# Kernel tuning notes

Hardware: AMD Instinct MI355X
Metric: run time of the kernel (lower is better)

The kernel has to match this reference:

```python
import jax, jax.numpy as jnp
import numpy as np

NUM_EMBEDDINGS = 1024
EMBEDDING_DIM = 256


def setup_inputs() -> dict:
    key = jax.random.key(0)
    kx, kw = jax.random.split(key)
    x = jax.random.normal(kx, (64, 32, 32, EMBEDDING_DIM), dtype=jnp.float32)
    # nn.Embedding default init: N(0, 1)
    embedding_weight = jax.random.normal(kw, (NUM_EMBEDDINGS, EMBEDDING_DIM), dtype=jnp.float32)
    return {"x": x, "embedding_weight": embedding_weight}


def reference(x, embedding_weight):
    D = embedding_weight.shape[1]
    x_flat = x.reshape(-1, D)  # [N, D]
    distances = (
        jnp.sum(x_flat * x_flat, axis=1, keepdims=True)
        + jnp.sum(embedding_weight * embedding_weight, axis=1)
        - 2.0 * jnp.matmul(x_flat, embedding_weight.T)
    )
    indices = jnp.argmin(distances, axis=1)  # [N]
    quantized = embedding_weight[indices].reshape(x.shape)
    return quantized, indices
```

## Files before the change

### kernel.cpp

```cpp
#include <hip/hip_runtime.h>


#define K_EMB  1024
#define D_DIM  256
#define N_ROWS 65536

typedef unsigned int u32;
typedef unsigned long long u64;
typedef __attribute__((ext_vector_type(8)))  _Float16 f16x8;
typedef __attribute__((ext_vector_type(4)))  _Float16 f16x4;
typedef __attribute__((ext_vector_type(16))) float    f32x16;

__device__ __forceinline__ u32 f32_sortable(float f) {
    u32 u = __float_as_uint(f);
    return u ^ ((u32)((int)u >> 31) | 0x80000000u);
}
__device__ __forceinline__ float f32_unsort(u32 u) {
    u32 v = (u & 0x80000000u) ? (u ^ 0x80000000u) : ~u;
    return __uint_as_float(v);
}

#define GLDS(gp, lp) __builtin_amdgcn_global_load_lds( \
    (const __attribute__((address_space(1))) void*)(gp), \
    (__attribute__((address_space(3))) void*)(lp), 16, 0, 0)

__global__ void vq_prep(const float* __restrict__ emb,
                        _Float16* __restrict__ ehi,
                        u32* __restrict__ cn2c,
                        float* __restrict__ cnormf) {
    int gid = blockIdx.x * 256 + threadIdx.x;
    int code = gid >> 6, lane = gid & 63;
    float4 v = ((const float4*)(emb + (size_t)code * D_DIM))[lane];
    f16x4 hv = {(_Float16)v.x, (_Float16)v.y, (_Float16)v.z, (_Float16)v.w};
    ((f16x4*)(ehi + (size_t)code * D_DIM))[lane] = hv;
    float s = v.x * v.x + v.y * v.y + v.z * v.z + v.w * v.w;
    #pragma unroll
    for (int off = 32; off > 0; off >>= 1) s += __shfl_down(s, off, 64);
    if (lane == 0) {
        float cn = 0.5f * s;
        cnormf[code] = cn;
        _Float16 ch = (_Float16)cn;
        _Float16 cl = (_Float16)(cn - (float)ch);
        union { _Float16 hh[2]; u32 uu; } pk;
        pk.hh[0] = (_Float16)(-(float)ch);
        pk.hh[1] = (_Float16)(-(float)cl);
        cn2c[code] = pk.uu;
    }
}

__global__ __launch_bounds__(512, 4) void vq_main(
    const float* __restrict__ x, const float* __restrict__ emb,
    const _Float16* __restrict__ eh, const u32* __restrict__ cn2c,
    const float* __restrict__ cnormf,
    float* __restrict__ outq, float* __restrict__ outi)
{
    __shared__ _Float16 T[2][2][8192];
    __shared__ u32 CNs[1024];
    __shared__ u32 xchg[2][128][3];
    __shared__ int winners[128];

    const int t = threadIdx.x, w = t >> 6, lane = t & 63;
    const int m = lane & 31, kh = lane >> 5;
    const int p = w >> 1;
    const int h = w & 1;
    const int blkrow = blockIdx.x * 128;
    const int kh4 = kh * 4;

    auto stage = [&](int c) {
        _Float16* dstb = &T[c & 1][h][0];
        const _Float16* srcb = eh + (size_t)(h * 512 + c * 32 + m) * D_DIM + kh * 8;
        #pragma unroll
        for (int i = 0; i < 4; i++) {
            int r = p * 4 + i;
            GLDS(srcb + r * 16, dstb + r * 512);
        }
    };

    stage(0);

    CNs[t] = cn2c[t];
    CNs[t + 512] = cn2c[t + 512];

    f16x8 bh[16];
    {
        char* xb = (char*)&T[1][0][0];
        #pragma unroll
        for (int k = 0; k < 2; k++) {
            #pragma unroll
            for (int i = 0; i < 8; i++) {
                int row = i * 8 + w;
                float4 v = *(const float4*)(
                    x + (size_t)(blkrow + k * 64 + row) * D_DIM + lane * 4);
                f16x4 hv = {(_Float16)v.x, (_Float16)v.y,
                            (_Float16)v.z, (_Float16)v.w};
                u32 byte = (u32)(row * 512 + lane * 8) ^ ((u32)(row & 7) << 4);
                *(f16x4*)(xb + byte) = hv;
            }
            __syncthreads();
            if ((p >> 1) == k) {
                int lr = (p & 1) * 32 + m;
                #pragma unroll
                for (int s = 0; s < 16; s++) {
                    u32 byte = (u32)(lr * 512 + s * 32 + kh * 16)
                             ^ ((u32)(lr & 7) << 4);
                    bh[s] = *(const f16x8*)(xb + byte);
                }
            }
            __syncthreads();
        }
    }
    f16x8 xe = {};
    if (kh == 0) { xe[0] = (_Float16)1.0f; xe[1] = (_Float16)1.0f; }

    u32 A1 = 0, A2 = 0, A3 = 0;

    auto t3 = [](u32& c1, u32& c2, u32& c3, u32 pv) {
        u32 u2 = c1 < pv ? c1 : pv;
        u32 u3 = c2 < pv ? c2 : pv;
        c1 = c1 > pv ? c1 : pv;
        c2 = u2 > c2 ? u2 : c2;
        c3 = u3 > c3 ? u3 : c3;
    };

    for (int c = 0; c < 16; ++c) {
        __builtin_amdgcn_sched_barrier(0);
        __builtin_amdgcn_s_barrier();
        if (c < 15) {
            stage(c + 1);
            asm volatile("s_waitcnt vmcnt(4)" ::: "memory");
        } else {
            asm volatile("s_waitcnt vmcnt(0)" ::: "memory");
        }
        __builtin_amdgcn_sched_barrier(0);
        __builtin_amdgcn_s_barrier();

        const f16x8* Af = (const f16x8*)&T[c & 1][h][0];
        union { u32 uu; _Float16 hh[2]; } uv;
        uv.uu = CNs[h * 512 + c * 32 + m];
        f16x8 e = {};
        e[0] = uv.hh[0]; e[1] = uv.hh[1];
        f32x16 a = {};
        __builtin_amdgcn_s_setprio(1);
        #pragma unroll
        for (int s = 0; s < 16; s++) {
            f16x8 fa = Af[(2 * s + kh) * 32 + m];
            a = __builtin_amdgcn_mfma_f32_32x32x16_f16(fa, bh[s], a, 0, 0, 0);
        }
        a = __builtin_amdgcn_mfma_f32_32x32x16_f16(e, xe, a, 0, 0, 0);
        __builtin_amdgcn_s_setprio(0);

        const u32 sbase = (u32)(h * 512 + c * 32) + kh4;
        #pragma unroll
        for (int r = 0; r < 16; r++) {
            u32 code = sbase + (r & 3) + 8 * (r >> 2);
            u32 pk = (f32_sortable(a[r]) & 0xFFFFFC00u) | code;
            t3(A1, A2, A3, pk);
        }
    }

    {
        u32 q1 = (u32)__shfl_xor((int)A1, 32, 64);
        u32 q2 = (u32)__shfl_xor((int)A2, 32, 64);
        u32 q3 = (u32)__shfl_xor((int)A3, 32, 64);
        t3(A1, A2, A3, q1); t3(A1, A2, A3, q2); t3(A1, A2, A3, q3);
    }

    if (kh == 0) {
        int ra = p * 32 + m;
        xchg[h][ra][0] = A1; xchg[h][ra][1] = A2; xchg[h][ra][2] = A3;
    }
    __syncthreads();

    const int lr = w * 16 + (lane & 15);
    u32 c1 = 0, c2 = 0, c3 = 0;
    #pragma unroll
    for (int hh = 0; hh < 2; hh++) {
        t3(c1, c2, c3, xchg[hh][lr][0]);
        t3(c1, c2, c3, xchg[hh][lr][1]);
        t3(c1, c2, c3, xchg[hh][lr][2]);
    }

    float s1f = f32_unsort(c1), s2f = f32_unsort(c2), s3f = f32_unsort(c3);
    u32 i1 = c1 & 1023u, i2 = c2 & 1023u, i3 = c3 & 1023u;
    const bool act = lane < 16;
    bool need = (s1f - s2f) <= 0.25f;
    if (act && !need) winners[lr] = (int)i1;
    u64 mask = __ballot(act && need);
    while (mask) {
        int r = __ffsll((unsigned long long)mask) - 1;
        mask &= mask - 1;
        int row = blkrow + w * 16 + r;
        u32 d1 = (u32)__shfl((int)i1, r, 64);
        u32 d2 = (u32)__shfl((int)i2, r, 64);
        u32 d3 = (u32)__shfl((int)i3, r, 64);
        float g3 = __shfl(s1f - s3f, r, 64);
        int ncand = (g3 <= 0.25f) ? 3 : 2;
        float4 xv = ((const float4*)(x + (size_t)row * D_DIM))[lane];
        float bs = -3.0e38f; int bi = 0x7fffffff;
        u32 cand[3] = {d1, d2, d3};
        for (int q = 0; q < ncand; q++) {
            int ccd = (int)cand[q];
            float4 ev = ((const float4*)(emb + (size_t)ccd * D_DIM))[lane];
            float d = xv.x * ev.x + xv.y * ev.y + xv.z * ev.z + xv.w * ev.w;
            #pragma unroll
            for (int dd = 1; dd < 64; dd <<= 1) d += __shfl_xor(d, dd, 64);
            float sc = d - cnormf[ccd];
            if (sc > bs || (sc == bs && ccd < bi)) { bs = sc; bi = ccd; }
        }
        if (lane == 0) winners[w * 16 + r] = bi;
    }

    if (act) outi[blkrow + lr] = (float)winners[lr];
    #pragma unroll 8
    for (int r = 0; r < 16; r++) {
        int idx = winners[w * 16 + r];
        int row = blkrow + w * 16 + r;
        float4 qv = ((const float4*)(emb + (size_t)idx * D_DIM))[lane];
        ((float4*)(outq + (size_t)row * D_DIM))[lane] = qv;
    }
}

extern "C" void kernel_launch(void* const* d_in, const int* in_sizes, int n_in,
                              void* d_out, int out_size, void* d_ws, size_t ws_size,
                              hipStream_t stream) {
    const float* x   = (const float*)d_in[0];
    const float* emb = (const float*)d_in[1];
    float* outq = (float*)d_out;
    float* outi = outq + (size_t)N_ROWS * D_DIM;

    _Float16* ehi = (_Float16*)d_ws;
    u32* cn2c = (u32*)(ehi + (size_t)K_EMB * D_DIM);
    float* cnormf = (float*)(cn2c + K_EMB);

    vq_prep<<<K_EMB / 4, 256, 0, stream>>>(emb, ehi, cn2c, cnormf);
    vq_main<<<N_ROWS / 128, 512, 0, stream>>>(x, emb, ehi, cn2c, cnormf,
                                              outq, outi);
}
```

Baseline: 155.1 us.

## Software-pipeline MFMA with top-3 selection and use float med3 top-3

Unrolls the codebook chunk loop by two with two accumulators, so the top-3 scan of the previous chunk runs while the MFMAs of the current chunk are issued. The unsigned sortable-key top-3 is replaced by a float top-3 built from fmed3/fmax on the raw float bits with the code index packed into the low mantissa bits, which removes the per-element sortable conversion. The cost is a second 16-float accumulator, which raises register pressure at 4 waves per SIMD, and the float comparison of index-packed values depends on those values not being negative or NaN.

```diff
diff --git a/kernel.cpp b/kernel.cpp
--- a/kernel.cpp
+++ b/kernel.cpp
@@ -10,15 +10,6 @@
 typedef __attribute__((ext_vector_type(8)))  _Float16 f16x8;
 typedef __attribute__((ext_vector_type(4)))  _Float16 f16x4;
 typedef __attribute__((ext_vector_type(16))) float    f32x16;
-
-__device__ __forceinline__ u32 f32_sortable(float f) {
-    u32 u = __float_as_uint(f);
-    return u ^ ((u32)((int)u >> 31) | 0x80000000u);
-}
-__device__ __forceinline__ float f32_unsort(u32 u) {
-    u32 v = (u & 0x80000000u) ? (u ^ 0x80000000u) : ~u;
-    return __uint_as_float(v);
-}
 
 #define GLDS(gp, lp) __builtin_amdgcn_global_load_lds( \
     (const __attribute__((address_space(1))) void*)(gp), \
@@ -65,6 +56,7 @@
     const int h = w & 1;
     const int blkrow = blockIdx.x * 128;
     const int kh4 = kh * 4;
+    const float NEGINF = __uint_as_float(0xFF800000u);
 
     auto stage = [&](int c) {
         _Float16* dstb = &T[c & 1][h][0];
@@ -112,34 +104,22 @@
     f16x8 xe = {};
     if (kh == 0) { xe[0] = (_Float16)1.0f; xe[1] = (_Float16)1.0f; }
 
-    u32 A1 = 0, A2 = 0, A3 = 0;
-
-    auto t3 = [](u32& c1, u32& c2, u32& c3, u32 pv) {
-        u32 u2 = c1 < pv ? c1 : pv;
-        u32 u3 = c2 < pv ? c2 : pv;
-        c1 = c1 > pv ? c1 : pv;
-        c2 = u2 > c2 ? u2 : c2;
-        c3 = u3 > c3 ? u3 : c3;
-    };
-
-    for (int c = 0; c < 16; ++c) {
-        __builtin_amdgcn_sched_barrier(0);
-        __builtin_amdgcn_s_barrier();
-        if (c < 15) {
-            stage(c + 1);
-            asm volatile("s_waitcnt vmcnt(4)" ::: "memory");
-        } else {
-            asm volatile("s_waitcnt vmcnt(0)" ::: "memory");
-        }
-        __builtin_amdgcn_sched_barrier(0);
-        __builtin_amdgcn_s_barrier();
-
-        const f16x8* Af = (const f16x8*)&T[c & 1][h][0];
+    float B1 = NEGINF, B2 = NEGINF, B3 = NEGINF;
+
+    auto t3f = [](float& c1, float& c2, float& c3, float pv) {
+        float n3 = __builtin_amdgcn_fmed3f(c2, pv, c3);
+        float n2 = __builtin_amdgcn_fmed3f(c1, pv, c2);
+        c1 = fmaxf(c1, pv);
+        c2 = n2; c3 = n3;
+    };
+
+    auto computeMF = [&](int buf, f32x16& a, int c) {
+        const f16x8* Af = (const f16x8*)&T[buf][h][0];
         union { u32 uu; _Float16 hh[2]; } uv;
         uv.uu = CNs[h * 512 + c * 32 + m];
         f16x8 e = {};
         e[0] = uv.hh[0]; e[1] = uv.hh[1];
-        f32x16 a = {};
+        a = (f32x16){};
         __builtin_amdgcn_s_setprio(1);
         #pragma unroll
         for (int s = 0; s < 16; s++) {
@@ -148,42 +128,73 @@
         }
         a = __builtin_amdgcn_mfma_f32_32x32x16_f16(e, xe, a, 0, 0, 0);
         __builtin_amdgcn_s_setprio(0);
-
+    };
+
+    auto top3p = [&](const f32x16& a, int c) {
         const u32 sbase = (u32)(h * 512 + c * 32) + kh4;
         #pragma unroll
         for (int r = 0; r < 16; r++) {
             u32 code = sbase + (r & 3) + 8 * (r >> 2);
-            u32 pk = (f32_sortable(a[r]) & 0xFFFFFC00u) | code;
-            t3(A1, A2, A3, pk);
-        }
-    }
+            u32 bits = (__float_as_uint(a[r]) & 0xFFFFFC00u) | code;
+            t3f(B1, B2, B3, __uint_as_float(bits));
+        }
+    };
+
+    f32x16 accA, accB;
+    for (int cc = 0; cc < 16; cc += 2) {
+        __builtin_amdgcn_sched_barrier(0);
+        __builtin_amdgcn_s_barrier();
+        stage(cc + 1);
+        asm volatile("s_waitcnt vmcnt(4)" ::: "memory");
+        __builtin_amdgcn_sched_barrier(0);
+        __builtin_amdgcn_s_barrier();
+        computeMF(0, accA, cc);
+        if (cc) top3p(accB, cc - 1);
+
+        __builtin_amdgcn_sched_barrier(0);
+        __builtin_amdgcn_s_barrier();
+        if (cc + 2 < 16) {
+            stage(cc + 2);
+            asm volatile("s_waitcnt vmcnt(4)" ::: "memory");
+        } else {
+            asm volatile("s_waitcnt vmcnt(0)" ::: "memory");
+        }
+        __builtin_amdgcn_sched_barrier(0);
+        __builtin_amdgcn_s_barrier();
+        computeMF(1, accB, cc + 1);
+        top3p(accA, cc);
+    }
+    top3p(accB, 15);
 
     {
-        u32 q1 = (u32)__shfl_xor((int)A1, 32, 64);
-        u32 q2 = (u32)__shfl_xor((int)A2, 32, 64);
-        u32 q3 = (u32)__shfl_xor((int)A3, 32, 64);
-        t3(A1, A2, A3, q1); t3(A1, A2, A3, q2); t3(A1, A2, A3, q3);
+        float q1 = __shfl_xor(B1, 32, 64);
+        float q2 = __shfl_xor(B2, 32, 64);
+        float q3 = __shfl_xor(B3, 32, 64);
+        t3f(B1, B2, B3, q1); t3f(B1, B2, B3, q2); t3f(B1, B2, B3, q3);
     }
 
     if (kh == 0) {
         int ra = p * 32 + m;
-        xchg[h][ra][0] = A1; xchg[h][ra][1] = A2; xchg[h][ra][2] = A3;
+        xchg[h][ra][0] = __float_as_uint(B1);
+        xchg[h][ra][1] = __float_as_uint(B2);
+        xchg[h][ra][2] = __float_as_uint(B3);
     }
     __syncthreads();
 
     const int lr = w * 16 + (lane & 15);
-    u32 c1 = 0, c2 = 0, c3 = 0;
+    float c1 = NEGINF, c2 = NEGINF, c3 = NEGINF;
     #pragma unroll
     for (int hh = 0; hh < 2; hh++) {
-        t3(c1, c2, c3, xchg[hh][lr][0]);
-        t3(c1, c2, c3, xchg[hh][lr][1]);
-        t3(c1, c2, c3, xchg[hh][lr][2]);
-    }
-
-    float s1f = f32_unsort(c1), s2f = f32_unsort(c2), s3f = f32_unsort(c3);
-    u32 i1 = c1 & 1023u, i2 = c2 & 1023u, i3 = c3 & 1023u;
+        t3f(c1, c2, c3, __uint_as_float(xchg[hh][lr][0]));
+        t3f(c1, c2, c3, __uint_as_float(xchg[hh][lr][1]));
+        t3f(c1, c2, c3, __uint_as_float(xchg[hh][lr][2]));
+    }
+
+    u32 i1 = __float_as_uint(c1) & 1023u;
+    u32 i2 = __float_as_uint(c2) & 1023u;
+    u32 i3 = __float_as_uint(c3) & 1023u;
     const bool act = lane < 16;
-    bool need = (s1f - s2f) <= 0.25f;
+    bool need = (c1 - c2) <= 0.25f;
     if (act && !need) winners[lr] = (int)i1;
     u64 mask = __ballot(act && need);
     while (mask) {
@@ -193,7 +204,7 @@
         u32 d1 = (u32)__shfl((int)i1, r, 64);
         u32 d2 = (u32)__shfl((int)i2, r, 64);
         u32 d3 = (u32)__shfl((int)i3, r, 64);
-        float g3 = __shfl(s1f - s3f, r, 64);
+        float g3 = __shfl(c1 - c3, r, 64);
         int ncand = (g3 <= 0.25f) ? 3 : 2;
         float4 xv = ((const float4*)(x + (size_t)row * D_DIM))[lane];
         float bs = -3.0e38f; int bi = 0x7fffffff;
```

Result: slower. 160.3 us (+3.3%).
